# Performance work log

Measured on AMD Instinct MI355X. Metric: run time of the kernel, lower is better.

The kernel has to match this reference:

```python
import jax, jax.numpy as jnp
import numpy as np

B, N, D, H = 256, 64, 128, 64

def _w(key, shape, fan_in):
    return jax.random.normal(key, shape, jnp.float32) * (1.0 / np.sqrt(fan_in))

def setup_inputs() -> dict:
    key = jax.random.key(0)
    ks = jax.random.split(key, 6)
    return {
        "observations": jax.random.normal(ks[0], (B, N, D), jnp.float32),
        "enc_w": _w(ks[1], (D, H), D), "enc_b": jnp.zeros((H,), jnp.float32),
        "gate_w1": _w(ks[2], (2 * H, H), 2 * H), "gate_b1": jnp.zeros((H,), jnp.float32),
        "gate_w2": _w(ks[3], (H, 1), H), "gate_b2": jnp.zeros((1,), jnp.float32),
        "msg_w1": _w(ks[4], (H, H), H), "msg_b1": jnp.zeros((H,), jnp.float32),
        "msg_w2": _w(ks[5], (H, H), H), "msg_b2": jnp.zeros((H,), jnp.float32),
    }

def reference(observations, enc_w, enc_b, gate_w1, gate_b1, gate_w2, gate_b2,
              msg_w1, msg_b1, msg_w2, msg_b2):
    # encoder: (B, N, H)
    enc = jax.nn.relu(observations @ enc_w + enc_b)
    h = enc.shape[-1]
    # gate layer 1 on concat([e_i, e_j]) == e_i @ W_top + e_j @ W_bot; avoids
    # materializing the (B, N, N, 2H) concat tensor.
    w_i, w_j = gate_w1[:h], gate_w1[h:]
    gi = enc @ w_i                       # (B, N, H) contribution of receiver i
    gj = enc @ w_j + gate_b1             # (B, N, H) contribution of sender j
    hid = jax.nn.relu(gi[:, :, None, :] + gj[:, None, :, :])   # (B, N, N, H)
    gates = jax.nn.sigmoid(jnp.squeeze(hid @ gate_w2, -1) + gate_b2[0])  # (B, N, N)
    # message_gen(encoded): identical for every i in the original loop
    msg = jax.nn.relu(enc @ msg_w1 + msg_b1) @ msg_w2 + msg_b2  # (B, N, H)
    # enhanced[b, i] = sum_j gates[b, i, j] * msg[b, j]
    enhanced = jnp.einsum('bij,bjh->bih', gates, msg)           # (B, N, H)
    return enhanced
```

## Files before the change

kernel.cpp:

```cpp
#include <hip/hip_runtime.h>

typedef float  f32x4  __attribute__((ext_vector_type(4)));
typedef short  bf16x8 __attribute__((ext_vector_type(8)));

#define Bb 256

__device__ __forceinline__ uint cvtpk(float lo, float hi) {
    uint r;
    asm("v_cvt_pk_bf16_f32 %0, %1, %2" : "=v"(r) : "v"(lo), "v"(hi));
    return r;
}
__device__ __forceinline__ ushort f2b1(float v) { return (ushort)cvtpk(v, v); }

union U8 { uint u[4]; bf16x8 v; };

__global__ __launch_bounds__(256) void gcm_prep(
    const float* __restrict__ obs, const float* __restrict__ enc_w,
    const float* __restrict__ gate_w1, const float* __restrict__ msg_w1,
    const float* __restrict__ msg_w2,
    ushort* __restrict__ obs_bf, ushort* __restrict__ wimg)
{
    const int bid = blockIdx.x, t = threadIdx.x;
    if (bid < 1024) {
        const int G  = bid * 256 + t;
        const int e0 = G * 8;
        const int b  = e0 >> 13;
        const int r  = (e0 >> 7) & 63;
        const int d0 = e0 & 127;
        const int ds = d0 ^ ((r & 7) << 3);
        const float* src = obs + (((size_t)b * 64 + r) * 128 + ds);
        float4 f0 = *(const float4*)src;
        float4 f1 = *(const float4*)(src + 4);
        uint4 o;
        o.x = cvtpk(f0.x, f0.y); o.y = cvtpk(f0.z, f0.w);
        o.z = cvtpk(f1.x, f1.y); o.w = cvtpk(f1.z, f1.w);
        *(uint4*)(obs_bf + e0) = o;
    } else {
        const int G  = (bid - 1024) * 256 + t;
        const int e0 = G * 8;
        float v[8];
        if (e0 < 8192) {
            const int n  = e0 >> 7;
            const int k0 = (e0 & 127) ^ ((n & 7) << 3);
            #pragma unroll
            for (int j = 0; j < 8; ++j) v[j] = enc_w[(k0 + j) * 64 + n];
        } else {
            const int e  = e0 - 8192;
            const int n  = e >> 6;
            const int k0 = (e & 63) ^ ((n & 7) << 3);
            const float* base; int col;
            if (n < 64)       { base = gate_w1;           col = n;       }
            else if (n < 128) { base = gate_w1 + 64 * 64; col = n - 64;  }
            else if (n < 192) { base = msg_w1;            col = n - 128; }
            else              { base = msg_w2;            col = n - 192; }
            #pragma unroll
            for (int j = 0; j < 8; ++j) v[j] = base[(k0 + j) * 64 + col];
        }
        uint4 o;
        o.x = cvtpk(v[0], v[1]); o.y = cvtpk(v[2], v[3]);
        o.z = cvtpk(v[4], v[5]); o.w = cvtpk(v[6], v[7]);
        *(uint4*)(wimg + e0) = o;
    }
}

__global__ __launch_bounds__(512, 4) void gcm_main(
    const ushort* __restrict__ obs_bf, const ushort* __restrict__ wimg,
    const float* __restrict__ enc_b, const float* __restrict__ gate_b1,
    const float* __restrict__ gate_w2, const float* __restrict__ gate_b2,
    const float* __restrict__ msg_b1, const float* __restrict__ msg_b2,
    float* __restrict__ out)
{
    const int bid  = blockIdx.x;
    const int bb   = bid >> 1;
    const int half = bid & 1;
    const int t    = threadIdx.x;
    const int lane = t & 63;
    const int wv   = t >> 6;
    const int lr   = lane & 15;
    const int lg   = lane >> 4;
    const int rt   = wv & 3;
    const int ch   = wv >> 2;

    __shared__ __align__(16) char arena[53248];
    ushort* s_enc    = (ushort*)(arena);
    ushort* s_msgh   = (ushort*)(arena + 8192);
    float*  s_gj     = (float*) (arena + 16384);
    ushort* s_msgT   = (ushort*)(arena + 32768);
    float*  s_gi     = (float*) (arena + 40960);
    ushort* s_gatesb = (ushort*)(arena + 49152);

    {
        const int arow = rt * 16 + lr;
        const ushort* ob = obs_bf + (size_t)bb * 8192 + arow * 128;
        bf16x8 a[4];
        #pragma unroll
        for (int ks = 0; ks < 4; ++ks)
            a[ks] = *(const bf16x8*)(ob + ((ks * 32 + lg * 8) ^ ((arow & 7) << 3)));
        f32x4 acc[2];
        acc[0] = (f32x4){0.f, 0.f, 0.f, 0.f};
        acc[1] = (f32x4){0.f, 0.f, 0.f, 0.f};
        #pragma unroll
        for (int jj = 0; jj < 2; ++jj) {
            const int n = ch * 32 + jj * 16 + lr;
            const ushort* wp = wimg + n * 128;
            #pragma unroll
            for (int ks = 0; ks < 4; ++ks) {
                bf16x8 bw = *(const bf16x8*)(wp + ((ks * 32 + lg * 8) ^ ((n & 7) << 3)));
                acc[jj] = __builtin_amdgcn_mfma_f32_16x16x32_bf16(a[ks], bw, acc[jj], 0, 0, 0);
            }
        }
        const int rb = rt * 16 + lg * 4;
        #pragma unroll
        for (int jj = 0; jj < 2; ++jj) {
            const int n = ch * 32 + jj * 16 + lr;
            const float be = enc_b[n];
            float v0 = fmaxf(acc[jj][0] + be, 0.f), v1 = fmaxf(acc[jj][1] + be, 0.f);
            float v2 = fmaxf(acc[jj][2] + be, 0.f), v3 = fmaxf(acc[jj][3] + be, 0.f);
            uint pA = cvtpk(v0, v1), pB = cvtpk(v2, v3);
            s_enc[((rb + 0) * 64 + n) ^ (((rb + 0) & 7) << 3)] = (ushort)pA;
            s_enc[((rb + 1) * 64 + n) ^ (((rb + 1) & 7) << 3)] = (ushort)(pA >> 16);
            s_enc[((rb + 2) * 64 + n) ^ (((rb + 2) & 7) << 3)] = (ushort)pB;
            s_enc[((rb + 3) * 64 + n) ^ (((rb + 3) & 7) << 3)] = (ushort)(pB >> 16);
        }
    }
    __syncthreads();

    {
        const int arow = rt * 16 + lr;
        bf16x8 a[2];
        #pragma unroll
        for (int ks = 0; ks < 2; ++ks)
            a[ks] = *(const bf16x8*)(s_enc + ((arow * 64 + ks * 32 + lg * 8) ^ ((arow & 7) << 3)));
        f32x4 acc[6];
        #pragma unroll
        for (int q = 0; q < 6; ++q) acc[q] = (f32x4){0.f, 0.f, 0.f, 0.f};
        #pragma unroll
        for (int q = 0; q < 6; ++q) {
            const int n = (ch * 6 + q) * 16 + lr;
            const ushort* wp = wimg + 8192 + n * 64;
            #pragma unroll
            for (int ks = 0; ks < 2; ++ks) {
                bf16x8 bw = *(const bf16x8*)(wp + ((ks * 32 + lg * 8) ^ ((n & 7) << 3)));
                acc[q] = __builtin_amdgcn_mfma_f32_16x16x32_bf16(a[ks], bw, acc[q], 0, 0, 0);
            }
        }
        const int rb = rt * 16 + lg * 4;
        #pragma unroll
        for (int q = 0; q < 6; ++q) {
            const int nfull = (ch * 6 + q) * 16;
            const int cc = nfull + lr;
            if (nfull < 64) {
                if ((rt >> 1) == half) {
                    const int lb = rb - half * 32;
                    #pragma unroll
                    for (int rr = 0; rr < 4; ++rr) {
                        const int row = lb + rr;
                        s_gi[(row * 64 + cc) ^ ((row & 7) << 2)] = acc[q][rr];
                    }
                }
            } else if (nfull < 128) {
                const float b1 = gate_b1[cc - 64];
                #pragma unroll
                for (int rr = 0; rr < 4; ++rr) {
                    const int row = rb + rr;
                    s_gj[(row * 64 + (cc - 64)) ^ ((row & 7) << 2)] = acc[q][rr] + b1;
                }
            } else {
                const float bm = msg_b1[cc - 128];
                float v0 = fmaxf(acc[q][0] + bm, 0.f), v1 = fmaxf(acc[q][1] + bm, 0.f);
                float v2 = fmaxf(acc[q][2] + bm, 0.f), v3 = fmaxf(acc[q][3] + bm, 0.f);
                uint pA = cvtpk(v0, v1), pB = cvtpk(v2, v3);
                const int c2 = cc - 128;
                s_msgh[((rb + 0) * 64 + c2) ^ (((rb + 0) & 7) << 3)] = (ushort)pA;
                s_msgh[((rb + 1) * 64 + c2) ^ (((rb + 1) & 7) << 3)] = (ushort)(pA >> 16);
                s_msgh[((rb + 2) * 64 + c2) ^ (((rb + 2) & 7) << 3)] = (ushort)pB;
                s_msgh[((rb + 3) * 64 + c2) ^ (((rb + 3) & 7) << 3)] = (ushort)(pB >> 16);
            }
        }
    }
    __syncthreads();

    {
        const int arow = rt * 16 + lr;
        bf16x8 a[2];
        #pragma unroll
        for (int ks = 0; ks < 2; ++ks)
            a[ks] = *(const bf16x8*)(s_msgh + ((arow * 64 + ks * 32 + lg * 8) ^ ((arow & 7) << 3)));
        #pragma unroll
        for (int jj = 0; jj < 2; ++jj) {
            const int n = 192 + ch * 32 + jj * 16 + lr;
            const ushort* wp = wimg + 8192 + n * 64;
            f32x4 acc = (f32x4){0.f, 0.f, 0.f, 0.f};
            #pragma unroll
            for (int ks = 0; ks < 2; ++ks) {
                bf16x8 bw = *(const bf16x8*)(wp + ((ks * 32 + lg * 8) ^ ((n & 7) << 3)));
                acc = __builtin_amdgcn_mfma_f32_16x16x32_bf16(a[ks], bw, acc, 0, 0, 0);
            }
            const int h  = ch * 32 + jj * 16 + lr;
            const int jb = rt * 16 + lg * 4;
            const float bm2 = msg_b2[h];
            uint pA = cvtpk(acc[0] + bm2, acc[1] + bm2);
            uint pB = cvtpk(acc[2] + bm2, acc[3] + bm2);
            const int e = (h * 64 + jb) ^ ((h & 7) << 3);
            *(uint*)(s_msgT + e)     = pA;
            *(uint*)(s_msgT + e + 2) = pB;
        }
    }

    {
        const int lrow0 = wv * 4;
        float ag[4] = {0.f, 0.f, 0.f, 0.f};
        #pragma unroll 4
        for (int h0 = 0; h0 < 64; h0 += 4) {
            float4 gj4 = *(const float4*)&s_gj[(lane * 64 + h0) ^ ((lane & 7) << 2)];
            const float4 w24 = *(const float4*)(gate_w2 + h0);
            #pragma unroll
            for (int r = 0; r < 4; ++r) {
                const int row = lrow0 + r;
                float4 gi4 = *(const float4*)&s_gi[(row * 64 + h0) ^ ((row & 7) << 2)];
                ag[r] = fmaf(fmaxf(gi4.x + gj4.x, 0.f), w24.x, ag[r]);
                ag[r] = fmaf(fmaxf(gi4.y + gj4.y, 0.f), w24.y, ag[r]);
                ag[r] = fmaf(fmaxf(gi4.z + gj4.z, 0.f), w24.z, ag[r]);
                ag[r] = fmaf(fmaxf(gi4.w + gj4.w, 0.f), w24.w, ag[r]);
            }
        }
        const float b2v = gate_b2[0];
        #pragma unroll
        for (int r = 0; r < 4; ++r) {
            const int row = lrow0 + r;
            const float g = 1.f / (1.f + __expf(-(ag[r] + b2v)));
            s_gatesb[(row * 64 + lane) ^ ((row & 7) << 3)] = f2b1(g);
        }
    }
    __syncthreads();

    {
        const int rtl = wv >> 2;
        const int ctl = wv & 3;
        f32x4 acc = (f32x4){0.f, 0.f, 0.f, 0.f};
        const int arow = rtl * 16 + lr;
        const int n = ctl * 16 + lr;
        #pragma unroll
        for (int ks = 0; ks < 2; ++ks) {
            const int k0 = ks * 32 + lg * 8;
            bf16x8 a  = *(const bf16x8*)(s_gatesb + ((arow * 64 + k0) ^ ((arow & 7) << 3)));
            bf16x8 bf = *(const bf16x8*)(s_msgT   + ((n * 64 + k0) ^ ((n & 7) << 3)));
            acc = __builtin_amdgcn_mfma_f32_16x16x32_bf16(a, bf, acc, 0, 0, 0);
        }
        const int rb = half * 32 + rtl * 16 + lg * 4;
        #pragma unroll
        for (int rr = 0; rr < 4; ++rr)
            out[((size_t)bb * 64 + rb + rr) * 64 + n] = acc[rr];
    }
}

__global__ __launch_bounds__(1024) void gcm_fb(
    const float* __restrict__ obs, const float* __restrict__ enc_w,
    const float* __restrict__ enc_b, const float* __restrict__ gate_w1,
    const float* __restrict__ gate_b1, const float* __restrict__ gate_w2,
    const float* __restrict__ gate_b2, const float* __restrict__ msg_w1,
    const float* __restrict__ msg_b1, const float* __restrict__ msg_w2,
    const float* __restrict__ msg_b2, float* __restrict__ out)
{
    const int bb   = blockIdx.x;
    const int t    = threadIdx.x;
    const int lane = t & 63;
    const int wv   = t >> 6;
    const int lr   = lane & 15;
    const int lg   = lane >> 4;
    const int rt   = wv & 3;
    const int ct   = wv >> 2;

    __shared__ __align__(16) ushort s_encwT[64 * 128];
    __shared__ __align__(16) ushort s_wT[256 * 64];
    __shared__ __align__(16) ushort s_enc[64 * 64];
    __shared__ __align__(16) ushort s_msgh[64 * 64];
    __shared__ __align__(16) ushort s_gatesb[64 * 64];
    __shared__ __align__(16) ushort s_msgT[64 * 64];
    __shared__ __align__(16) float  s_gi[64 * 64];
    __shared__ __align__(16) float  s_gj[64 * 64];
    __shared__ __align__(16) float  s_w2[64];

    float4 pf[8];
    {
        const float* ob = obs + ((size_t)bb * 64 + rt * 16 + lr) * 128 + lg * 8;
        #pragma unroll
        for (int ks = 0; ks < 4; ++ks) {
            pf[2 * ks]     = *(const float4*)(ob + ks * 32);
            pf[2 * ks + 1] = *(const float4*)(ob + ks * 32 + 4);
        }
    }
    if (t < 64) s_w2[t] = gate_w2[t];
    #pragma unroll
    for (int it = 0; it < 2; ++it) {
        const int g  = t + it * 1024;
        const int k  = g >> 4;
        const int n0 = (g & 15) * 4;
        float4 w4 = *(const float4*)(enc_w + k * 64 + n0);
        uint pA = cvtpk(w4.x, w4.y), pB = cvtpk(w4.z, w4.w);
        s_encwT[((n0 + 0) * 128 + k) ^ (((n0 + 0) & 7) << 3)] = (ushort)pA;
        s_encwT[((n0 + 1) * 128 + k) ^ (((n0 + 1) & 7) << 3)] = (ushort)(pA >> 16);
        s_encwT[((n0 + 2) * 128 + k) ^ (((n0 + 2) & 7) << 3)] = (ushort)pB;
        s_encwT[((n0 + 3) * 128 + k) ^ (((n0 + 3) & 7) << 3)] = (ushort)(pB >> 16);
    }
    bf16x8 afrag[4];
    #pragma unroll
    for (int ks = 0; ks < 4; ++ks) {
        U8 u;
        u.u[0] = cvtpk(pf[2 * ks].x,     pf[2 * ks].y);
        u.u[1] = cvtpk(pf[2 * ks].z,     pf[2 * ks].w);
        u.u[2] = cvtpk(pf[2 * ks + 1].x, pf[2 * ks + 1].y);
        u.u[3] = cvtpk(pf[2 * ks + 1].z, pf[2 * ks + 1].w);
        afrag[ks] = u.v;
    }
    float4 pfw[4];
    {
        const int k  = t >> 4;
        const int n0 = (t & 15) * 4;
        pfw[0] = *(const float4*)(gate_w1 + k * 64 + n0);
        pfw[1] = *(const float4*)(gate_w1 + (64 + k) * 64 + n0);
        pfw[2] = *(const float4*)(msg_w1 + k * 64 + n0);
        pfw[3] = *(const float4*)(msg_w2 + k * 64 + n0);
    }
    __syncthreads();
    {
        f32x4 acc = (f32x4){0.f, 0.f, 0.f, 0.f};
        const int n = ct * 16 + lr;
        #pragma unroll
        for (int ks = 0; ks < 4; ++ks) {
            const int k0 = ks * 32 + lg * 8;
            bf16x8 bf = *(const bf16x8*)(s_encwT + ((n * 128 + k0) ^ ((n & 7) << 3)));
            acc = __builtin_amdgcn_mfma_f32_16x16x32_bf16(afrag[ks], bf, acc, 0, 0, 0);
        }
        #pragma unroll
        for (int it = 0; it < 4; ++it) {
            const int k  = t >> 4;
            const int n0 = it * 64 + (t & 15) * 4;
            uint pA = cvtpk(pfw[it].x, pfw[it].y), pB = cvtpk(pfw[it].z, pfw[it].w);
            s_wT[((n0 + 0) * 64 + k) ^ (((n0 + 0) & 7) << 3)] = (ushort)pA;
            s_wT[((n0 + 1) * 64 + k) ^ (((n0 + 1) & 7) << 3)] = (ushort)(pA >> 16);
            s_wT[((n0 + 2) * 64 + k) ^ (((n0 + 2) & 7) << 3)] = (ushort)pB;
            s_wT[((n0 + 3) * 64 + k) ^ (((n0 + 3) & 7) << 3)] = (ushort)(pB >> 16);
        }
        const float be = enc_b[n];
        float v0 = fmaxf(acc[0] + be, 0.f), v1 = fmaxf(acc[1] + be, 0.f);
        float v2 = fmaxf(acc[2] + be, 0.f), v3 = fmaxf(acc[3] + be, 0.f);
        uint pA = cvtpk(v0, v1), pB = cvtpk(v2, v3);
        const int rb = rt * 16 + lg * 4;
        s_enc[((rb + 0) * 64 + n) ^ (((rb + 0) & 7) << 3)] = (ushort)pA;
        s_enc[((rb + 1) * 64 + n) ^ (((rb + 1) & 7) << 3)] = (ushort)(pA >> 16);
        s_enc[((rb + 2) * 64 + n) ^ (((rb + 2) & 7) << 3)] = (ushort)pB;
        s_enc[((rb + 3) * 64 + n) ^ (((rb + 3) & 7) << 3)] = (ushort)(pB >> 16);
    }
    __syncthreads();
    {
        f32x4 acc[3];
        #pragma unroll
        for (int q = 0; q < 3; ++q) acc[q] = (f32x4){0.f, 0.f, 0.f, 0.f};
        const int arow = rt * 16 + lr;
        #pragma unroll
        for (int ks = 0; ks < 2; ++ks) {
            const int k0 = ks * 32 + lg * 8;
            bf16x8 a = *(const bf16x8*)(s_enc + ((arow * 64 + k0) ^ ((arow & 7) << 3)));
            #pragma unroll
            for (int q = 0; q < 3; ++q) {
                const int n = (ct * 3 + q) * 16 + lr;
                bf16x8 bf = *(const bf16x8*)(s_wT + ((n * 64 + k0) ^ ((n & 7) << 3)));
                acc[q] = __builtin_amdgcn_mfma_f32_16x16x32_bf16(a, bf, acc[q], 0, 0, 0);
            }
        }
        const int rb = rt * 16 + lg * 4;
        #pragma unroll
        for (int q = 0; q < 3; ++q) {
            const int nfull = (ct * 3 + q) * 16;
            const int cc = nfull + lr;
            if (nfull < 64) {
                #pragma unroll
                for (int rr = 0; rr < 4; ++rr) {
                    const int row = rb + rr;
                    s_gi[(row * 64 + cc) ^ ((row & 7) << 2)] = acc[q][rr];
                }
            } else if (nfull < 128) {
                const float b1 = gate_b1[cc - 64];
                #pragma unroll
                for (int rr = 0; rr < 4; ++rr) {
                    const int row = rb + rr;
                    s_gj[(row * 64 + (cc - 64)) ^ ((row & 7) << 2)] = acc[q][rr] + b1;
                }
            } else {
                const float bm = msg_b1[cc - 128];
                float v0 = fmaxf(acc[q][0] + bm, 0.f), v1 = fmaxf(acc[q][1] + bm, 0.f);
                float v2 = fmaxf(acc[q][2] + bm, 0.f), v3 = fmaxf(acc[q][3] + bm, 0.f);
                uint pA = cvtpk(v0, v1), pB = cvtpk(v2, v3);
                const int c2 = cc - 128;
                s_msgh[((rb + 0) * 64 + c2) ^ (((rb + 0) & 7) << 3)] = (ushort)pA;
                s_msgh[((rb + 1) * 64 + c2) ^ (((rb + 1) & 7) << 3)] = (ushort)(pA >> 16);
                s_msgh[((rb + 2) * 64 + c2) ^ (((rb + 2) & 7) << 3)] = (ushort)pB;
                s_msgh[((rb + 3) * 64 + c2) ^ (((rb + 3) & 7) << 3)] = (ushort)(pB >> 16);
            }
        }
    }
    __syncthreads();
    {
        f32x4 acc = (f32x4){0.f, 0.f, 0.f, 0.f};
        const int arow = rt * 16 + lr;
        const int nn3 = 192 + ct * 16 + lr;
        #pragma unroll
        for (int ks = 0; ks < 2; ++ks) {
            const int k0 = ks * 32 + lg * 8;
            bf16x8 a = *(const bf16x8*)(s_msgh + ((arow * 64 + k0) ^ ((arow & 7) << 3)));
            bf16x8 bf = *(const bf16x8*)(s_wT + ((nn3 * 64 + k0) ^ ((nn3 & 7) << 3)));
            acc = __builtin_amdgcn_mfma_f32_16x16x32_bf16(a, bf, acc, 0, 0, 0);
        }
        const int h  = ct * 16 + lr;
        const int jb = rt * 16 + lg * 4;
        const float bm2 = msg_b2[h];
        uint pA = cvtpk(acc[0] + bm2, acc[1] + bm2);
        uint pB = cvtpk(acc[2] + bm2, acc[3] + bm2);
        const int e = (h * 64 + jb) ^ ((h & 7) << 3);
        *(uint*)(s_msgT + e)     = pA;
        *(uint*)(s_msgT + e + 2) = pB;
    }
    {
        const int row0g = wv * 4;
        float ag[4] = {0.f, 0.f, 0.f, 0.f};
        #pragma unroll 4
        for (int h0 = 0; h0 < 64; h0 += 4) {
            float4 gj4 = *(const float4*)&s_gj[(lane * 64 + h0) ^ ((lane & 7) << 2)];
            float4 w24 = *(const float4*)&s_w2[h0];
            #pragma unroll
            for (int r = 0; r < 4; ++r) {
                const int row = row0g + r;
                float4 gi4 = *(const float4*)&s_gi[(row * 64 + h0) ^ ((row & 7) << 2)];
                ag[r] = fmaf(fmaxf(gi4.x + gj4.x, 0.f), w24.x, ag[r]);
                ag[r] = fmaf(fmaxf(gi4.y + gj4.y, 0.f), w24.y, ag[r]);
                ag[r] = fmaf(fmaxf(gi4.z + gj4.z, 0.f), w24.z, ag[r]);
                ag[r] = fmaf(fmaxf(gi4.w + gj4.w, 0.f), w24.w, ag[r]);
            }
        }
        const float b2v = gate_b2[0];
        #pragma unroll
        for (int r = 0; r < 4; ++r) {
            const int row = row0g + r;
            const float g = 1.f / (1.f + __expf(-(ag[r] + b2v)));
            s_gatesb[(row * 64 + lane) ^ ((row & 7) << 3)] = f2b1(g);
        }
    }
    __syncthreads();
    {
        const int rtl = wv >> 2;
        const int ctl = wv & 3;
        f32x4 acc = (f32x4){0.f, 0.f, 0.f, 0.f};
        const int arow = rtl * 16 + lr;
        const int n = ctl * 16 + lr;
        #pragma unroll
        for (int ks = 0; ks < 2; ++ks) {
            const int k0 = ks * 32 + lg * 8;
            bf16x8 a  = *(const bf16x8*)(s_gatesb + ((arow * 64 + k0) ^ ((arow & 7) << 3)));
            bf16x8 bf = *(const bf16x8*)(s_msgT   + ((n * 64 + k0) ^ ((n & 7) << 3)));
            acc = __builtin_amdgcn_mfma_f32_16x16x32_bf16(a, bf, acc, 0, 0, 0);
        }
        const int rb = rtl * 16 + lg * 4;
        #pragma unroll
        for (int rr = 0; rr < 4; ++rr)
            out[((size_t)bb * 64 + rb + rr) * 64 + n] = acc[rr];
    }
}

extern "C" void kernel_launch(void* const* d_in, const int* in_sizes, int n_in,
                              void* d_out, int out_size, void* d_ws, size_t ws_size,
                              hipStream_t stream) {
    const float* obs     = (const float*)d_in[0];
    const float* enc_w   = (const float*)d_in[1];
    const float* enc_b   = (const float*)d_in[2];
    const float* gate_w1 = (const float*)d_in[3];
    const float* gate_b1 = (const float*)d_in[4];
    const float* gate_w2 = (const float*)d_in[5];
    const float* gate_b2 = (const float*)d_in[6];
    const float* msg_w1  = (const float*)d_in[7];
    const float* msg_b1  = (const float*)d_in[8];
    const float* msg_w2  = (const float*)d_in[9];
    const float* msg_b2  = (const float*)d_in[10];
    float* out = (float*)d_out;

    const size_t obs_elems = (size_t)Bb * 64 * 128;
    const size_t w_elems   = 24576;
    const size_t need = (obs_elems + w_elems) * sizeof(ushort);
    if (ws_size >= need) {
        ushort* obs_bf = (ushort*)d_ws;
        ushort* wimg   = obs_bf + obs_elems;
        gcm_prep<<<1036, 256, 0, stream>>>(obs, enc_w, gate_w1, msg_w1, msg_w2,
                                           obs_bf, wimg);
        gcm_main<<<2 * Bb, 512, 0, stream>>>(obs_bf, wimg, enc_b, gate_b1,
                                             gate_w2, gate_b2, msg_b1, msg_b2, out);
    } else {
        gcm_fb<<<Bb, 1024, 0, stream>>>(obs, enc_w, enc_b, gate_w1, gate_b1,
                                        gate_w2, gate_b2, msg_w1, msg_b1,
                                        msg_w2, msg_b2, out);
    }
}
```

Before: 24.56 us.

## Stage weights into LDS asynchronously and move gate-i activations to bf16 workspace

At kernel start the gate and message weight image is copied straight from global memory into LDS with global_load_lds, so the later MFMA stages read B operands from LDS instead of global memory. The receiver-side gate activations (gi) are written as bf16 to a global workspace and read back with wave-uniform (readfirstlane) addresses. The sender-side activations (gj) are held in LDS as bf16 and unpacked into 64 registers per lane, which restructures the gate-score loop. In exchange, LDS use per block grows, which can cut the number of resident blocks per CU. Register pressure also rises, bf16 rounding is added to gi and gj, and the design relies on global-memory writes being visible to reads within the same block.

After: 22.43 us. 1.09x faster.

```diff
diff --git a/kernel.cpp b/kernel.cpp
--- a/kernel.cpp
+++ b/kernel.cpp
@@ -11,6 +11,14 @@
     return r;
 }
 __device__ __forceinline__ ushort f2b1(float v) { return (ushort)cvtpk(v, v); }
+__device__ __forceinline__ float bflo(uint u) { return __uint_as_float(u << 16); }
+__device__ __forceinline__ float bfhi(uint u) { return __uint_as_float(u & 0xffff0000u); }
+
+__device__ __forceinline__ void gl_lds16(const void* g, void* l) {
+    __builtin_amdgcn_global_load_lds(
+        (const __attribute__((address_space(1))) unsigned int*)g,
+        (__attribute__((address_space(3))) unsigned int*)l, 16, 0, 0);
+}
 
 union U8 { uint u[4]; bf16x8 v; };
 
@@ -68,7 +76,7 @@
     const float* __restrict__ enc_b, const float* __restrict__ gate_b1,
     const float* __restrict__ gate_w2, const float* __restrict__ gate_b2,
     const float* __restrict__ msg_b1, const float* __restrict__ msg_b2,
-    float* __restrict__ out)
+    ushort* __restrict__ gi_ws, float* __restrict__ out)
 {
     const int bid  = blockIdx.x;
     const int bb   = bid >> 1;
@@ -81,13 +89,19 @@
     const int rt   = wv & 3;
     const int ch   = wv >> 2;
 
-    __shared__ __align__(16) char arena[53248];
-    ushort* s_enc    = (ushort*)(arena);
-    ushort* s_msgh   = (ushort*)(arena + 8192);
-    float*  s_gj     = (float*) (arena + 16384);
+    __shared__ __align__(16) char arena[61440];
+    ushort* s_wT     = (ushort*)(arena);
+    ushort* s_enc    = (ushort*)(arena + 32768);
     ushort* s_msgT   = (ushort*)(arena + 32768);
-    float*  s_gi     = (float*) (arena + 40960);
-    ushort* s_gatesb = (ushort*)(arena + 49152);
+    ushort* s_msgh   = (ushort*)(arena + 40960);
+    ushort* s_gjb    = (ushort*)(arena + 49152);
+    ushort* s_gatesb = (ushort*)(arena + 57344);
+
+    #pragma unroll
+    for (int i = 0; i < 4; ++i) {
+        const int idx = wv * 4 + i;
+        gl_lds16(wimg + 8192 + idx * 512 + lane * 8, arena + idx * 1024);
+    }
 
     {
         const int arow = rt * 16 + lr;
@@ -127,21 +141,20 @@
 
     {
         const int arow = rt * 16 + lr;
-        bf16x8 a[2];
+        bf16x8 a2[2];
         #pragma unroll
         for (int ks = 0; ks < 2; ++ks)
-            a[ks] = *(const bf16x8*)(s_enc + ((arow * 64 + ks * 32 + lg * 8) ^ ((arow & 7) << 3)));
+            a2[ks] = *(const bf16x8*)(s_enc + ((arow * 64 + ks * 32 + lg * 8) ^ ((arow & 7) << 3)));
         f32x4 acc[6];
         #pragma unroll
         for (int q = 0; q < 6; ++q) acc[q] = (f32x4){0.f, 0.f, 0.f, 0.f};
         #pragma unroll
         for (int q = 0; q < 6; ++q) {
             const int n = (ch * 6 + q) * 16 + lr;
-            const ushort* wp = wimg + 8192 + n * 64;
             #pragma unroll
             for (int ks = 0; ks < 2; ++ks) {
-                bf16x8 bw = *(const bf16x8*)(wp + ((ks * 32 + lg * 8) ^ ((n & 7) << 3)));
-                acc[q] = __builtin_amdgcn_mfma_f32_16x16x32_bf16(a[ks], bw, acc[q], 0, 0, 0);
+                bf16x8 bw = *(const bf16x8*)(s_wT + ((n * 64 + ks * 32 + lg * 8) ^ ((n & 7) << 3)));
+                acc[q] = __builtin_amdgcn_mfma_f32_16x16x32_bf16(a2[ks], bw, acc[q], 0, 0, 0);
             }
         }
         const int rb = rt * 16 + lg * 4;
@@ -151,19 +164,16 @@
             const int cc = nfull + lr;
             if (nfull < 64) {
                 if ((rt >> 1) == half) {
-                    const int lb = rb - half * 32;
                     #pragma unroll
-                    for (int rr = 0; rr < 4; ++rr) {
-                        const int row = lb + rr;
-                        s_gi[(row * 64 + cc) ^ ((row & 7) << 2)] = acc[q][rr];
-                    }
+                    for (int rr = 0; rr < 4; ++rr)
+                        gi_ws[(size_t)bb * 4096 + (rb + rr) * 64 + cc] = f2b1(acc[q][rr]);
                 }
             } else if (nfull < 128) {
                 const float b1 = gate_b1[cc - 64];
                 #pragma unroll
                 for (int rr = 0; rr < 4; ++rr) {
                     const int row = rb + rr;
-                    s_gj[(row * 64 + (cc - 64)) ^ ((row & 7) << 2)] = acc[q][rr] + b1;
+                    s_gjb[(row * 64 + (cc - 64)) ^ ((row & 7) << 3)] = f2b1(acc[q][rr] + b1);
                 }
             } else {
                 const float bm = msg_b1[cc - 128];
@@ -182,19 +192,18 @@
 
     {
         const int arow = rt * 16 + lr;
-        bf16x8 a[2];
+        bf16x8 a3[2];
         #pragma unroll
         for (int ks = 0; ks < 2; ++ks)
-            a[ks] = *(const bf16x8*)(s_msgh + ((arow * 64 + ks * 32 + lg * 8) ^ ((arow & 7) << 3)));
+            a3[ks] = *(const bf16x8*)(s_msgh + ((arow * 64 + ks * 32 + lg * 8) ^ ((arow & 7) << 3)));
         #pragma unroll
         for (int jj = 0; jj < 2; ++jj) {
             const int n = 192 + ch * 32 + jj * 16 + lr;
-            const ushort* wp = wimg + 8192 + n * 64;
             f32x4 acc = (f32x4){0.f, 0.f, 0.f, 0.f};
             #pragma unroll
             for (int ks = 0; ks < 2; ++ks) {
-                bf16x8 bw = *(const bf16x8*)(wp + ((ks * 32 + lg * 8) ^ ((n & 7) << 3)));
-                acc = __builtin_amdgcn_mfma_f32_16x16x32_bf16(a[ks], bw, acc, 0, 0, 0);
+                bf16x8 bw = *(const bf16x8*)(s_wT + ((n * 64 + ks * 32 + lg * 8) ^ ((n & 7) << 3)));
+                acc = __builtin_amdgcn_mfma_f32_16x16x32_bf16(a3[ks], bw, acc, 0, 0, 0);
             }
             const int h  = ch * 32 + jj * 16 + lr;
             const int jb = rt * 16 + lg * 4;
@@ -209,27 +218,30 @@
 
     {
         const int lrow0 = wv * 4;
-        float ag[4] = {0.f, 0.f, 0.f, 0.f};
-        #pragma unroll 4
-        for (int h0 = 0; h0 < 64; h0 += 4) {
-            float4 gj4 = *(const float4*)&s_gj[(lane * 64 + h0) ^ ((lane & 7) << 2)];
-            const float4 w24 = *(const float4*)(gate_w2 + h0);
-            #pragma unroll
-            for (int r = 0; r < 4; ++r) {
-                const int row = lrow0 + r;
-                float4 gi4 = *(const float4*)&s_gi[(row * 64 + h0) ^ ((row & 7) << 2)];
-                ag[r] = fmaf(fmaxf(gi4.x + gj4.x, 0.f), w24.x, ag[r]);
-                ag[r] = fmaf(fmaxf(gi4.y + gj4.y, 0.f), w24.y, ag[r]);
-                ag[r] = fmaf(fmaxf(gi4.z + gj4.z, 0.f), w24.z, ag[r]);
-                ag[r] = fmaf(fmaxf(gi4.w + gj4.w, 0.f), w24.w, ag[r]);
-            }
+        float gjv[64];
+        #pragma unroll
+        for (int c8 = 0; c8 < 8; ++c8) {
+            uint4 p = *(const uint4*)(s_gjb + ((lane * 64 + c8 * 8) ^ ((lane & 7) << 3)));
+            gjv[c8 * 8 + 0] = bflo(p.x); gjv[c8 * 8 + 1] = bfhi(p.x);
+            gjv[c8 * 8 + 2] = bflo(p.y); gjv[c8 * 8 + 3] = bfhi(p.y);
+            gjv[c8 * 8 + 4] = bflo(p.z); gjv[c8 * 8 + 5] = bfhi(p.z);
+            gjv[c8 * 8 + 6] = bflo(p.w); gjv[c8 * 8 + 7] = bfhi(p.w);
         }
         const float b2v = gate_b2[0];
         #pragma unroll
         for (int r = 0; r < 4; ++r) {
-            const int row = lrow0 + r;
-            const float g = 1.f / (1.f + __expf(-(ag[r] + b2v)));
-            s_gatesb[(row * 64 + lane) ^ ((row & 7) << 3)] = f2b1(g);
+            const int lrow = lrow0 + r;
+            const int grow = __builtin_amdgcn_readfirstlane(half * 32 + lrow);
+            const uint* gip = (const uint*)(gi_ws + (size_t)bb * 4096 + grow * 64);
+            float acc = 0.f;
+            #pragma unroll
+            for (int c = 0; c < 32; ++c) {
+                const uint p = gip[c];
+                acc = fmaf(fmaxf(bflo(p) + gjv[2 * c],     0.f), gate_w2[2 * c],     acc);
+                acc = fmaf(fmaxf(bfhi(p) + gjv[2 * c + 1], 0.f), gate_w2[2 * c + 1], acc);
+            }
+            const float g = 1.f / (1.f + __expf(-(acc + b2v)));
+            s_gatesb[(lrow * 64 + lane) ^ ((lrow & 7) << 3)] = f2b1(g);
         }
     }
     __syncthreads();
@@ -243,9 +255,9 @@
         #pragma unroll
         for (int ks = 0; ks < 2; ++ks) {
             const int k0 = ks * 32 + lg * 8;
-            bf16x8 a  = *(const bf16x8*)(s_gatesb + ((arow * 64 + k0) ^ ((arow & 7) << 3)));
-            bf16x8 bf = *(const bf16x8*)(s_msgT   + ((n * 64 + k0) ^ ((n & 7) << 3)));
-            acc = __builtin_amdgcn_mfma_f32_16x16x32_bf16(a, bf, acc, 0, 0, 0);
+            bf16x8 a5 = *(const bf16x8*)(s_gatesb + ((arow * 64 + k0) ^ ((arow & 7) << 3)));
+            bf16x8 b5 = *(const bf16x8*)(s_msgT   + ((n * 64 + k0) ^ ((n & 7) << 3)));
+            acc = __builtin_amdgcn_mfma_f32_16x16x32_bf16(a5, b5, acc, 0, 0, 0);
         }
         const int rb = half * 32 + rtl * 16 + lg * 4;
         #pragma unroll
@@ -485,14 +497,17 @@
 
     const size_t obs_elems = (size_t)Bb * 64 * 128;
     const size_t w_elems   = 24576;
-    const size_t need = (obs_elems + w_elems) * sizeof(ushort);
+    const size_t gi_elems  = (size_t)Bb * 64 * 64;
+    const size_t need = (obs_elems + w_elems + gi_elems) * sizeof(ushort);
     if (ws_size >= need) {
         ushort* obs_bf = (ushort*)d_ws;
         ushort* wimg   = obs_bf + obs_elems;
+        ushort* gi_ws  = wimg + w_elems;
         gcm_prep<<<1036, 256, 0, stream>>>(obs, enc_w, gate_w1, msg_w1, msg_w2,
                                            obs_bf, wimg);
         gcm_main<<<2 * Bb, 512, 0, stream>>>(obs_bf, wimg, enc_b, gate_b1,
-                                             gate_w2, gate_b2, msg_b1, msg_b2, out);
+                                             gate_w2, gate_b2, msg_b1, msg_b2,
+                                             gi_ws, out);
     } else {
         gcm_fb<<<Bb, 1024, 0, stream>>>(obs, enc_w, enc_b, gate_w1, gate_b1,
                                         gate_w2, gate_b2, msg_w1, msg_b1,
```
